# Performance work log

Measured on AMD Instinct MI355X. Metric: run time of the kernel, lower is better.

## Reference

```python
import jax, jax.numpy as jnp
import numpy as np

B, T, D = 2, 2048, 2048
H, KVH = 16, 4
HD = D // H            # 128
HALF = HD // 2         # 64
EPS = 1e-6


def zc_rmsnorm(x, scale):
    # zero-centred RMSNorm: (1+scale) * x / rms(x), rms in fp32
    rms = jnp.sqrt(jnp.mean(x.astype(jnp.float32) ** 2, axis=-1, keepdims=True) + EPS)
    return ((1.0 + scale) * x / rms).astype(x.dtype)


def apply_rope(x, cos, sin):
    # x: [B, h, T, HD]; cos/sin: [T, HALF]
    t = x.shape[2]
    c = cos[:t][None, None, :, :]
    s = sin[:t][None, None, :, :]
    x1, x2 = x[..., :HALF], x[..., HALF:]
    return jnp.concatenate([x1 * c - x2 * s, x2 * c + x1 * s], axis=-1)


def setup_inputs() -> dict:
    key = jax.random.key(0)
    ks = jax.random.split(key, 8)
    std = 0.02
    res_std = 0.02 / np.sqrt(2 * 24)
    q_input = jax.random.normal(ks[0], (B, T, D), jnp.float32)
    kv_input = jax.random.normal(ks[1], (B, T, D), jnp.float32)
    mask = jnp.tril(jnp.ones((T, T), bool))[None, None, :, :]
    inv_freq = 1.0 / (10000.0 ** (jnp.arange(0, HALF, dtype=jnp.float32) / HALF))
    ang = jnp.arange(T, dtype=jnp.float32)[:, None] * inv_freq[None, :]
    cos, sin = jnp.cos(ang), jnp.sin(ang)
    Wq = jax.random.normal(ks[2], (D, D), jnp.float32) * std
    Wk = jax.random.normal(ks[3], (D, KVH * HD), jnp.float32) * std
    Wv = jax.random.normal(ks[4], (D, KVH * HD), jnp.float32) * std
    q_scale = jnp.zeros((HD,), jnp.float32)
    k_scale = jnp.zeros((HD,), jnp.float32)
    Wo = jax.random.normal(ks[5], (D, D), jnp.float32) * res_std
    return {"q_input": q_input, "kv_input": kv_input, "mask": mask,
            "cos": cos, "sin": sin, "Wq": Wq, "Wk": Wk, "Wv": Wv,
            "q_scale": q_scale, "k_scale": k_scale, "Wo": Wo}


def reference(q_input, kv_input, mask, cos, sin, Wq, Wk, Wv, q_scale, k_scale, Wo):
    b = q_input.shape[0]
    q = (q_input @ Wq).reshape(b, -1, H, HD).transpose(0, 2, 1, 3)      # [B,H,T,HD]
    k = (kv_input @ Wk).reshape(b, -1, KVH, HD).transpose(0, 2, 1, 3)   # [B,KVH,T,HD]
    v = (kv_input @ Wv).reshape(b, -1, KVH, HD).transpose(0, 2, 1, 3)
    q = zc_rmsnorm(q, q_scale)
    k = zc_rmsnorm(k, k_scale)
    rep = H // KVH
    k = jnp.repeat(k, rep, axis=1)
    v = jnp.repeat(v, rep, axis=1)
    q = apply_rope(q, cos, sin)
    k = apply_rope(k, cos, sin)
    scale = jnp.sqrt(jnp.float32(HD))
    scores = jnp.einsum('bhqd,bhkd->bhqk', q, k) / scale                # [B,H,T,T]
    scores = jnp.where(mask, scores, jnp.finfo(scores.dtype).min)
    attn = jax.nn.softmax(scores, axis=-1)
    out = jnp.einsum('bhqk,bhkd->bhqd', attn, v)
    out = out.transpose(0, 2, 1, 3).reshape(b, -1, D)
    return out @ Wo
```

## Files before the change

### kernel.cpp

```cpp
#include <hip/hip_runtime.h>

#define NB 2
#define NT 2048
#define ND 2048
#define NH 16
#define NKVH 4
#define NHD 128
#define NHALF 64
#define NREP (NH / NKVH)
#define MFIX 12.0f

typedef __bf16 bf16x8 __attribute__((ext_vector_type(8)));
typedef unsigned short u16x8 __attribute__((ext_vector_type(8)));
typedef float f32x4 __attribute__((ext_vector_type(4)));

__device__ __forceinline__ unsigned short f2b(float f) {
  union { float f; unsigned int u; } v; v.f = f;
  unsigned int r = v.u + 0x7FFFu + ((v.u >> 16) & 1u);
  return (unsigned short)(r >> 16);
}
__device__ __forceinline__ float b2f(unsigned short h) {
  union { unsigned int u; float f; } v; v.u = ((unsigned int)h) << 16;
  return v.f;
}

__device__ __forceinline__ void glds16(const unsigned short* g, unsigned short* l) {
  __builtin_amdgcn_global_load_lds(
      (__attribute__((address_space(1))) unsigned int*)(unsigned long long)g,
      (__attribute__((address_space(3))) unsigned int*)(unsigned int)(unsigned long long)l,
      16, 0, 0);
}

__global__ __launch_bounds__(256) void f2bf(const float* __restrict__ in,
                                            unsigned short* __restrict__ out) {
  const size_t i = (size_t)(blockIdx.x * 256 + threadIdx.x) * 8;
  float4 a = *(const float4*)(in + i);
  float4 b = *(const float4*)(in + i + 4);
  u16x8 r;
  r[0] = f2b(a.x); r[1] = f2b(a.y); r[2] = f2b(a.z); r[3] = f2b(a.w);
  r[4] = f2b(b.x); r[5] = f2b(b.y); r[6] = f2b(b.z); r[7] = f2b(b.w);
  *(u16x8*)(out + i) = r;
}

__global__ __launch_bounds__(256) void wtrans(const float* __restrict__ in,
                                              unsigned short* __restrict__ out,
                                              int K, int N) {
  __shared__ float tile[32][33];
  const int k0 = blockIdx.y * 32, n0 = blockIdx.x * 32;
  const int x = threadIdx.x & 31, y8 = threadIdx.x >> 5;
#pragma unroll
  for (int j = 0; j < 4; ++j) {
    const int y = y8 + j * 8;
    tile[y][x] = in[(size_t)(k0 + y) * N + n0 + x];
  }
  __syncthreads();
#pragma unroll
  for (int j = 0; j < 4; ++j) {
    const int y = y8 + j * 8;
    out[(size_t)(n0 + y) * K + k0 + x] = f2b(tile[x][y]);
  }
}

__global__ __launch_bounds__(256) void gemm128(const unsigned short* __restrict__ A,
                                               const unsigned short* __restrict__ Bt,
                                               float* __restrict__ C,
                                               int M, int N, int K) {
  __shared__ unsigned short As[2][128 * 32];
  __shared__ unsigned short Bs[2][128 * 32];
  const int tid = threadIdx.x;
  const int wave = tid >> 6, lane = tid & 63;
  const int wm = wave >> 1, wn = wave & 1;
  const int quad = lane >> 4, c = lane & 15;

  const int gx = gridDim.x;
  const int nwg = gx * gridDim.y;
  int lin = blockIdx.y * gx + blockIdx.x;
  lin = (lin & 7) * (nwg >> 3) + (lin >> 3);
  const int m0 = (lin / gx) * 128, n0 = (lin % gx) * 128;

  const unsigned short* pa0 = A + (size_t)(m0 + wave * 16 + (lane >> 2)) * K + (lane & 3) * 8;
  const unsigned short* pa1 = pa0 + (size_t)64 * K;
  const unsigned short* pb0 = Bt + (size_t)(n0 + wave * 16 + (lane >> 2)) * K + (lane & 3) * 8;
  const unsigned short* pb1 = pb0 + (size_t)64 * K;

  f32x4 acc[4][4] = {};

  const int nsteps = K >> 5;
  int cur = 0;
  glds16(pa0, &As[0][(wave * 16) * 32]);
  glds16(pa1, &As[0][(64 + wave * 16) * 32]);
  glds16(pb0, &Bs[0][(wave * 16) * 32]);
  glds16(pb1, &Bs[0][(64 + wave * 16) * 32]);
  __syncthreads();

  for (int t = 0; t < nsteps; ++t) {
    if (t + 1 < nsteps) {
      const int kn = (t + 1) << 5;
      glds16(pa0 + kn, &As[cur ^ 1][(wave * 16) * 32]);
      glds16(pa1 + kn, &As[cur ^ 1][(64 + wave * 16) * 32]);
      glds16(pb0 + kn, &Bs[cur ^ 1][(wave * 16) * 32]);
      glds16(pb1 + kn, &Bs[cur ^ 1][(64 + wave * 16) * 32]);
    }
    bf16x8 af[4];
#pragma unroll
    for (int sm = 0; sm < 4; ++sm)
      af[sm] = *(const bf16x8*)&As[cur][(wm * 64 + sm * 16 + c) * 32 + quad * 8];
#pragma unroll
    for (int sn = 0; sn < 4; ++sn) {
      bf16x8 bfr = *(const bf16x8*)&Bs[cur][(wn * 64 + sn * 16 + c) * 32 + quad * 8];
#pragma unroll
      for (int sm = 0; sm < 4; ++sm)
        acc[sm][sn] = __builtin_amdgcn_mfma_f32_16x16x32_bf16(af[sm], bfr, acc[sm][sn], 0, 0, 0);
    }
    __syncthreads();
    cur ^= 1;
  }

#pragma unroll
  for (int sm = 0; sm < 4; ++sm)
#pragma unroll
    for (int sn = 0; sn < 4; ++sn) {
      const int row = m0 + wm * 64 + sm * 16 + quad * 4;
      const int col = n0 + wn * 64 + sn * 16 + c;
#pragma unroll
      for (int r = 0; r < 4; ++r)
        C[(size_t)(row + r) * N + col] = acc[sm][sn][r];
    }
}

__global__ __launch_bounds__(256) void rmsnorm_rope(const float* __restrict__ in,
                                                    unsigned short* __restrict__ out,
                                                    const float* __restrict__ scale,
                                                    const float* __restrict__ cosp,
                                                    const float* __restrict__ sinp,
                                                    int nh, int instride, float outscale) {
  const int wid = blockIdx.x * 4 + (threadIdx.x >> 6);
  const int lane = threadIdx.x & 63;
  const int h = wid % nh;
  const int t = (wid / nh) % NT;
  const int b = wid / (nh * NT);
  const float* x = in + (size_t)(b * NT + t) * instride + h * NHD;
  float x1 = x[lane], x2 = x[lane + NHALF];
  float ss = x1 * x1 + x2 * x2;
#pragma unroll
  for (int m = 1; m < 64; m <<= 1) ss += __shfl_xor(ss, m, 64);
  const float inv = 1.0f / sqrtf(ss * (1.0f / NHD) + 1e-6f);
  const float n1 = (1.0f + scale[lane]) * x1 * inv;
  const float n2 = (1.0f + scale[lane + NHALF]) * x2 * inv;
  const float cc = cosp[t * NHALF + lane], s = sinp[t * NHALF + lane];
  const size_t ob = (((size_t)b * nh + h) * NT + t) * NHD;
  out[ob + lane] = f2b((n1 * cc - n2 * s) * outscale);
  out[ob + lane + NHALF] = f2b((n2 * cc + n1 * s) * outscale);
}

__global__ __launch_bounds__(256) void vtrans(const float* __restrict__ in,
                                              unsigned short* __restrict__ out,
                                              int instride) {
  __shared__ float tile[32][33];
  const int bg = blockIdx.z;
  const int b = bg >> 2, g = bg & 3;
  const int t0 = blockIdx.x * 32, d0 = blockIdx.y * 32;
  const int x = threadIdx.x & 31, y8 = threadIdx.x >> 5;
#pragma unroll
  for (int j = 0; j < 4; ++j) {
    const int y = y8 + j * 8;
    tile[y][x] = in[(size_t)(b * NT + t0 + y) * instride + g * NHD + d0 + x];
  }
  __syncthreads();
#pragma unroll
  for (int j = 0; j < 4; ++j) {
    const int y = y8 + j * 8;
    out[((size_t)bg * NHD + d0 + y) * NT + t0 + x] = f2b(tile[x][y]);
  }
}

__global__ __launch_bounds__(256, 3) void attn64(const unsigned short* __restrict__ Qh,
                                                 const unsigned short* __restrict__ Kh,
                                                 const unsigned short* __restrict__ Vtg,
                                                 unsigned short* __restrict__ O) {
  __shared__ unsigned short Kt[64 * 132];
  __shared__ unsigned short Vt[128 * 68];
  __shared__ unsigned short Pt[64 * 68];
  const int bh = blockIdx.x;
  const int b = bh / NH, h = bh % NH, g = h / NREP;
  const int y = blockIdx.y;
  const int a = y & 7, bb = y >> 3;
  const int qt = (bb == 0) ? a : (bb == 1) ? a + 8 : (bb == 2) ? 31 - a : 23 - a;
  const int tid = threadIdx.x;
  const int w = tid >> 6, lane = tid & 63;
  const int quad = lane >> 4, c = lane & 15;

  bf16x8 qf[4];
  {
    const unsigned short* qp =
        Qh + ((size_t)(b * NH + h) * NT + qt * 64 + w * 16 + c) * NHD + quad * 8;
#pragma unroll
    for (int ch = 0; ch < 4; ++ch) qf[ch] = *(const bf16x8*)(qp + ch * 32);
  }

  f32x4 acc_o[8] = {};
  float lsum[4] = {0.f, 0.f, 0.f, 0.f};
  const size_t kbase = (size_t)(b * NKVH + g) * NT * NHD;
  const size_t vbase = (size_t)(b * NKVH + g) * NHD * NT;
  const int nkt = qt + 1;

  u16x8 kreg[4], vreg[4];
#pragma unroll
  for (int j = 0; j < 4; ++j) {
    const int f = j * 256 + tid;
    kreg[j] = *(const u16x8*)&Kh[kbase + (size_t)(f >> 4) * NHD + (f & 15) * 8];
    vreg[j] = *(const u16x8*)&Vtg[vbase + (size_t)(f >> 3) * NT + (f & 7) * 8];
  }

  for (int kt = 0; kt < nkt; ++kt) {
#pragma unroll
    for (int j = 0; j < 4; ++j) {
      const int f = j * 256 + tid;
      *(u16x8*)&Kt[(f >> 4) * 132 + (f & 15) * 8] = kreg[j];
      *(u16x8*)&Vt[(f >> 3) * 68 + (f & 7) * 8] = vreg[j];
    }
    __syncthreads();

    if (kt + 1 < nkt) {
      const int k0 = (kt + 1) * 64;
#pragma unroll
      for (int j = 0; j < 4; ++j) {
        const int f = j * 256 + tid;
        kreg[j] = *(const u16x8*)&Kh[kbase + (size_t)(k0 + (f >> 4)) * NHD + (f & 15) * 8];
        vreg[j] = *(const u16x8*)&Vtg[vbase + (size_t)(f >> 3) * NT + k0 + (f & 7) * 8];
      }
    }

    f32x4 s[4] = {};
#pragma unroll
    for (int n = 0; n < 4; ++n)
#pragma unroll
      for (int ch = 0; ch < 4; ++ch) {
        bf16x8 kf = *(const bf16x8*)&Kt[(n * 16 + c) * 132 + ch * 32 + quad * 8];
        s[n] = __builtin_amdgcn_mfma_f32_16x16x32_bf16(qf[ch], kf, s[n], 0, 0, 0);
      }

    const bool dmask = (kt == qt);
#pragma unroll
    for (int r = 0; r < 4; ++r) {
      float v0 = s[0][r], v1 = s[1][r], v2 = s[2][r], v3 = s[3][r];
      const int lrow = w * 16 + quad * 4 + r;
      if (dmask) {
        if (c > lrow) v0 = -1e30f;
        if (16 + c > lrow) v1 = -1e30f;
        if (32 + c > lrow) v2 = -1e30f;
        if (48 + c > lrow) v3 = -1e30f;
      }
      const float p0 = __expf(v0 - MFIX), p1 = __expf(v1 - MFIX);
      const float p2 = __expf(v2 - MFIX), p3 = __expf(v3 - MFIX);
      lsum[r] += (p0 + p1) + (p2 + p3);
      Pt[lrow * 68 + c] = f2b(p0);
      Pt[lrow * 68 + 16 + c] = f2b(p1);
      Pt[lrow * 68 + 32 + c] = f2b(p2);
      Pt[lrow * 68 + 48 + c] = f2b(p3);
    }

#pragma unroll
    for (int kc2 = 0; kc2 < 2; ++kc2) {
      bf16x8 pf = *(const bf16x8*)&Pt[(w * 16 + c) * 68 + kc2 * 32 + quad * 8];
#pragma unroll
      for (int n2 = 0; n2 < 8; ++n2) {
        bf16x8 vf = *(const bf16x8*)&Vt[(n2 * 16 + c) * 68 + kc2 * 32 + quad * 8];
        acc_o[n2] = __builtin_amdgcn_mfma_f32_16x16x32_bf16(pf, vf, acc_o[n2], 0, 0, 0);
      }
    }
    __syncthreads();
  }

#pragma unroll
  for (int r = 0; r < 4; ++r) {
    float l = lsum[r];
    l += __shfl_xor(l, 1, 64);
    l += __shfl_xor(l, 2, 64);
    l += __shfl_xor(l, 4, 64);
    l += __shfl_xor(l, 8, 64);
    lsum[r] = l;
  }

#pragma unroll
  for (int r = 0; r < 4; ++r) {
    const float invl = 1.0f / lsum[r];
    const int qrow = qt * 64 + w * 16 + quad * 4 + r;
    unsigned short* op = O + ((size_t)(b * NT + qrow) * NH + h) * NHD + c;
#pragma unroll
    for (int n2 = 0; n2 < 8; ++n2) op[n2 * 16] = f2b(acc_o[n2][r] * invl);
  }
}

extern "C" void kernel_launch(void* const* d_in, const int* in_sizes, int n_in,
                              void* d_out, int out_size, void* d_ws, size_t ws_size,
                              hipStream_t stream) {
  (void)in_sizes; (void)n_in; (void)out_size; (void)ws_size;
  const float* q_input  = (const float*)d_in[0];
  const float* kv_input = (const float*)d_in[1];
  const float* cosp = (const float*)d_in[3];
  const float* sinp = (const float*)d_in[4];
  const float* Wq = (const float*)d_in[5];
  const float* Wk = (const float*)d_in[6];
  const float* Wv = (const float*)d_in[7];
  const float* q_scale = (const float*)d_in[8];
  const float* k_scale = (const float*)d_in[9];
  const float* Wo = (const float*)d_in[10];
  float* out = (float*)d_out;

  char* p = (char*)d_ws;
  float* Q32  = (float*)p; p += (size_t)NB * NT * ND * 4;
  float* KVp  = (float*)p; p += (size_t)NB * NT * 1024 * 4;
  unsigned short* Qb16  = (unsigned short*)p; p += (size_t)NB * NT * ND * 2;
  unsigned short* KVb16 = (unsigned short*)p; p += (size_t)NB * NT * ND * 2;
  unsigned short* Kh  = (unsigned short*)p; p += (size_t)NB * NKVH * NT * NHD * 2;
  unsigned short* Vtg = (unsigned short*)p; p += (size_t)NB * NKVH * NT * NHD * 2;
  unsigned short* Wqt  = (unsigned short*)p; p += (size_t)ND * ND * 2;
  unsigned short* WkvT = (unsigned short*)p; p += (size_t)1024 * ND * 2;
  unsigned short* Wot  = (unsigned short*)p; p += (size_t)ND * ND * 2;
  unsigned short* Ob = Qb16;
  unsigned short* Qh = KVb16;

  const dim3 blk(256);
  const int M = NB * NT;

  f2bf<<<dim3(M * ND / 2048), blk, 0, stream>>>(q_input, Qb16);
  f2bf<<<dim3(M * ND / 2048), blk, 0, stream>>>(kv_input, KVb16);

  wtrans<<<dim3(ND / 32, ND / 32), blk, 0, stream>>>(Wq, Wqt, ND, ND);
  wtrans<<<dim3(512 / 32, ND / 32), blk, 0, stream>>>(Wk, WkvT, ND, 512);
  wtrans<<<dim3(512 / 32, ND / 32), blk, 0, stream>>>(Wv, WkvT + (size_t)512 * ND, ND, 512);
  wtrans<<<dim3(ND / 32, ND / 32), blk, 0, stream>>>(Wo, Wot, ND, ND);

  gemm128<<<dim3(ND / 128, M / 128), blk, 0, stream>>>(Qb16, Wqt, Q32, M, ND, ND);
  gemm128<<<dim3(1024 / 128, M / 128), blk, 0, stream>>>(KVb16, WkvT, KVp, M, 1024, ND);

  rmsnorm_rope<<<dim3(NB * NT * NH / 4), blk, 0, stream>>>(Q32, Qh, q_scale, cosp, sinp,
                                                           NH, ND, 0.08838834764831845f);
  rmsnorm_rope<<<dim3(NB * NT * NKVH / 4), blk, 0, stream>>>(KVp, Kh, k_scale, cosp, sinp,
                                                             NKVH, 1024, 1.0f);
  vtrans<<<dim3(NT / 32, NHD / 32, NB * NKVH), blk, 0, stream>>>(KVp + 512, Vtg, 1024);

  attn64<<<dim3(NB * NH, 32), blk, 0, stream>>>(Qh, Kh, Vtg, Ob);

  gemm128<<<dim3(ND / 128, M / 128), blk, 0, stream>>>(Ob, Wot, out, M, ND, ND);
}
```

Measured before the change: 385.8 us.

## Widen GEMM K-tile to 64 with swizzled LDS and merge Q/KV projections

The GEMM core now stages 128x64 K-slices per step instead of 128x32, with an XOR swizzle on the LDS layout meant to avoid bank conflicts. This halves the number of barrier and loop iterations. The Q and KV projection GEMMs are merged into one 768-workgroup launch, which removes a launch and the tail effect of the smaller KV GEMM. LDS per block doubles to 64KB, which may lower occupancy.

```diff
diff --git a/kernel.cpp b/kernel.cpp
--- a/kernel.cpp
+++ b/kernel.cpp
@@ -61,71 +61,111 @@
   }
 }
 
+__device__ __forceinline__ void gemm_core(const unsigned short* __restrict__ A,
+                                          const unsigned short* __restrict__ Bt,
+                                          float* __restrict__ C,
+                                          int N, int K, int m0, int n0,
+                                          unsigned short* As, unsigned short* Bs) {
+  const int tid = threadIdx.x;
+  const int wave = tid >> 6, lane = tid & 63;
+  const int wm = wave >> 1, wn = wave & 1;
+  const int quad = lane >> 4, c = lane & 15;
+  const int lr = lane >> 3;
+  const int gsw = ((lane & 7) ^ lr) * 8;
+
+  const unsigned short* pa[4];
+  const unsigned short* pb[4];
+  unsigned short* da[4];
+  unsigned short* db[4];
+#pragma unroll
+  for (int j = 0; j < 4; ++j) {
+    const int rb = j * 32 + wave * 8;
+    pa[j] = A + (size_t)(m0 + rb + lr) * K + gsw;
+    pb[j] = Bt + (size_t)(n0 + rb + lr) * K + gsw;
+    da[j] = As + rb * 64;
+    db[j] = Bs + rb * 64;
+  }
+
+  f32x4 acc[4][4] = {};
+  const int nsteps = K >> 6;
+  int cur = 0;
+
+#pragma unroll
+  for (int j = 0; j < 4; ++j) { glds16(pa[j], da[j]); glds16(pb[j], db[j]); }
+  __syncthreads();
+
+  for (int t = 0; t < nsteps; ++t) {
+    const int nxt = (cur ^ 1) * (128 * 64);
+    if (t + 1 < nsteps) {
+      const int kn = (t + 1) << 6;
+#pragma unroll
+      for (int j = 0; j < 4; ++j) {
+        glds16(pa[j] + kn, da[j] + nxt);
+        glds16(pb[j] + kn, db[j] + nxt);
+      }
+    }
+    const unsigned short* Ab = As + cur * (128 * 64);
+    const unsigned short* Bb = Bs + cur * (128 * 64);
+#pragma unroll
+    for (int kk = 0; kk < 2; ++kk) {
+      const int g = ((kk * 4 + quad) ^ (c & 7)) * 8;
+      bf16x8 af[4];
+#pragma unroll
+      for (int sm = 0; sm < 4; ++sm)
+        af[sm] = *(const bf16x8*)&Ab[(wm * 64 + sm * 16 + c) * 64 + g];
+#pragma unroll
+      for (int sn = 0; sn < 4; ++sn) {
+        bf16x8 bfr = *(const bf16x8*)&Bb[(wn * 64 + sn * 16 + c) * 64 + g];
+#pragma unroll
+        for (int sm = 0; sm < 4; ++sm)
+          acc[sm][sn] = __builtin_amdgcn_mfma_f32_16x16x32_bf16(af[sm], bfr, acc[sm][sn], 0, 0, 0);
+      }
+    }
+    __syncthreads();
+    cur ^= 1;
+  }
+
+#pragma unroll
+  for (int sm = 0; sm < 4; ++sm)
+#pragma unroll
+    for (int sn = 0; sn < 4; ++sn) {
+      const int row = m0 + wm * 64 + sm * 16 + quad * 4;
+      const int col = n0 + wn * 64 + sn * 16 + c;
+#pragma unroll
+      for (int r = 0; r < 4; ++r)
+        C[(size_t)(row + r) * N + col] = acc[sm][sn][r];
+    }
+}
+
 __global__ __launch_bounds__(256) void gemm128(const unsigned short* __restrict__ A,
                                                const unsigned short* __restrict__ Bt,
                                                float* __restrict__ C,
                                                int M, int N, int K) {
-  __shared__ unsigned short As[2][128 * 32];
-  __shared__ unsigned short Bs[2][128 * 32];
-  const int tid = threadIdx.x;
-  const int wave = tid >> 6, lane = tid & 63;
-  const int wm = wave >> 1, wn = wave & 1;
-  const int quad = lane >> 4, c = lane & 15;
-
+  __shared__ unsigned short As[2 * 128 * 64];
+  __shared__ unsigned short Bs[2 * 128 * 64];
   const int gx = gridDim.x;
   const int nwg = gx * gridDim.y;
   int lin = blockIdx.y * gx + blockIdx.x;
   lin = (lin & 7) * (nwg >> 3) + (lin >> 3);
-  const int m0 = (lin / gx) * 128, n0 = (lin % gx) * 128;
-
-  const unsigned short* pa0 = A + (size_t)(m0 + wave * 16 + (lane >> 2)) * K + (lane & 3) * 8;
-  const unsigned short* pa1 = pa0 + (size_t)64 * K;
-  const unsigned short* pb0 = Bt + (size_t)(n0 + wave * 16 + (lane >> 2)) * K + (lane & 3) * 8;
-  const unsigned short* pb1 = pb0 + (size_t)64 * K;
-
-  f32x4 acc[4][4] = {};
-
-  const int nsteps = K >> 5;
-  int cur = 0;
-  glds16(pa0, &As[0][(wave * 16) * 32]);
-  glds16(pa1, &As[0][(64 + wave * 16) * 32]);
-  glds16(pb0, &Bs[0][(wave * 16) * 32]);
-  glds16(pb1, &Bs[0][(64 + wave * 16) * 32]);
-  __syncthreads();
-
-  for (int t = 0; t < nsteps; ++t) {
-    if (t + 1 < nsteps) {
-      const int kn = (t + 1) << 5;
-      glds16(pa0 + kn, &As[cur ^ 1][(wave * 16) * 32]);
-      glds16(pa1 + kn, &As[cur ^ 1][(64 + wave * 16) * 32]);
-      glds16(pb0 + kn, &Bs[cur ^ 1][(wave * 16) * 32]);
-      glds16(pb1 + kn, &Bs[cur ^ 1][(64 + wave * 16) * 32]);
-    }
-    bf16x8 af[4];
-#pragma unroll
-    for (int sm = 0; sm < 4; ++sm)
-      af[sm] = *(const bf16x8*)&As[cur][(wm * 64 + sm * 16 + c) * 32 + quad * 8];
-#pragma unroll
-    for (int sn = 0; sn < 4; ++sn) {
-      bf16x8 bfr = *(const bf16x8*)&Bs[cur][(wn * 64 + sn * 16 + c) * 32 + quad * 8];
-#pragma unroll
-      for (int sm = 0; sm < 4; ++sm)
-        acc[sm][sn] = __builtin_amdgcn_mfma_f32_16x16x32_bf16(af[sm], bfr, acc[sm][sn], 0, 0, 0);
-    }
-    __syncthreads();
-    cur ^= 1;
-  }
-
-#pragma unroll
-  for (int sm = 0; sm < 4; ++sm)
-#pragma unroll
-    for (int sn = 0; sn < 4; ++sn) {
-      const int row = m0 + wm * 64 + sm * 16 + quad * 4;
-      const int col = n0 + wn * 64 + sn * 16 + c;
-#pragma unroll
-      for (int r = 0; r < 4; ++r)
-        C[(size_t)(row + r) * N + col] = acc[sm][sn][r];
-    }
+  gemm_core(A, Bt, C, N, K, (lin / gx) * 128, (lin % gx) * 128, As, Bs);
+}
+
+__global__ __launch_bounds__(256) void gemm_qkv(const unsigned short* __restrict__ Aq,
+                                                const unsigned short* __restrict__ Wq,
+                                                float* __restrict__ Cq,
+                                                const unsigned short* __restrict__ Akv,
+                                                const unsigned short* __restrict__ Wkv,
+                                                float* __restrict__ Ckv) {
+  __shared__ unsigned short As[2 * 128 * 64];
+  __shared__ unsigned short Bs[2 * 128 * 64];
+  int lin = blockIdx.x;
+  lin = (lin & 7) * 96 + (lin >> 3);
+  if (lin < 512) {
+    gemm_core(Aq, Wq, Cq, 2048, 2048, (lin >> 4) * 128, (lin & 15) * 128, As, Bs);
+  } else {
+    const int l2 = lin - 512;
+    gemm_core(Akv, Wkv, Ckv, 1024, 2048, (l2 >> 3) * 128, (l2 & 7) * 128, As, Bs);
+  }
 }
 
 __global__ __launch_bounds__(256) void rmsnorm_rope(const float* __restrict__ in,
@@ -332,8 +372,7 @@
   wtrans<<<dim3(512 / 32, ND / 32), blk, 0, stream>>>(Wv, WkvT + (size_t)512 * ND, ND, 512);
   wtrans<<<dim3(ND / 32, ND / 32), blk, 0, stream>>>(Wo, Wot, ND, ND);
 
-  gemm128<<<dim3(ND / 128, M / 128), blk, 0, stream>>>(Qb16, Wqt, Q32, M, ND, ND);
-  gemm128<<<dim3(1024 / 128, M / 128), blk, 0, stream>>>(KVb16, WkvT, KVp, M, 1024, ND);
+  gemm_qkv<<<dim3(768), blk, 0, stream>>>(Qb16, Wqt, Q32, KVb16, WkvT, KVp);
 
   rmsnorm_rope<<<dim3(NB * NT * NH / 4), blk, 0, stream>>>(Q32, Qh, q_scale, cosp, sinp,
                                                            NH, ND, 0.08838834764831845f);
```

After: 366.4 us. 5.0% less time.
